# Kernel tuning notes

Measured on AMD Instinct MI355X. Metric: run time of the kernel, lower is better.

Reference implementation:

```python
import jax, jax.numpy as jnp
import numpy as np

N_PARENT = 50000   # parent voxels
C_IN = 256
C_OUT = 256
FANOUT = 8         # children per parent (kernel 2, stride 2 generative conv)
N_TGT = 200000     # number of ground-truth-occupied child indices


def setup_inputs() -> dict:
    key = jax.random.key(0)
    k_fea, k_wup, k_wcls, k_idx = jax.random.split(key, 4)
    fea = jax.random.normal(k_fea, (N_PARENT, C_IN), dtype=jnp.float32)
    W_up = jax.random.normal(k_wup, (FANOUT, C_IN, C_OUT), dtype=jnp.float32) * (1.0 / np.sqrt(C_IN))
    b_up = jnp.zeros((C_OUT,), dtype=jnp.float32)
    W_cls = jax.random.normal(k_wcls, (C_OUT, 1), dtype=jnp.float32) * (1.0 / np.sqrt(C_OUT))
    b_cls = jnp.zeros((1,), dtype=jnp.float32)
    # kernel_map in-indices into the upsampled coordinate set (GT-occupied children)
    target_idx = jax.random.randint(k_idx, (N_TGT,), 0, N_PARENT * FANOUT, dtype=jnp.int64)
    return {"fea": fea, "W_up": W_up, "b_up": b_up, "W_cls": W_cls,
            "b_cls": b_cls, "target_idx": target_idx}


def reference(fea, W_up, b_up, W_cls, b_cls, target_idx):
    # upsample_block: generative transposed sparse conv. Every parent voxel emits
    # FANOUT children, each via its own [C_IN, C_OUT] kernel slice.
    # [N, C_IN] x [K, C_IN, C_OUT] -> [N, K, C_OUT] -> [N*K, C_OUT]
    fea_up = jnp.einsum('nc,kcd->nkd', fea, W_up).reshape(-1, W_up.shape[2]) + b_up
    # classify_block: 1-channel existence logit
    exist = fea_up @ W_cls + b_cls                      # [N*K, 1]
    # keep = exist > 0 (computed under no_grad in torch)
    keep = jax.lax.stop_gradient(exist[:, 0]) > 0       # [N*K] bool
    # kernel_map target scatter: target[curr_in] = 1
    n_up = fea_up.shape[0]
    target = jnp.zeros((n_up,), dtype=jnp.bool_).at[target_idx].set(True)
    keep = keep | target                                # training: keep |= target
    # MinkowskiPruning(fea, keep): jit-compatible masking instead of compaction
    fea_pruned = jnp.where(keep[:, None], fea_up, jnp.zeros((), fea_up.dtype))
    return fea_pruned, exist, target
```

## Files before the change

kernel.cpp:

```cpp
#include <hip/hip_runtime.h>
#include <hip/hip_bf16.h>

#define N_PARENT 50000
#define C_IN     256
#define C_OUT    256
#define FANOUT   8
#define N_TGT    200000
#define N_UP     (N_PARENT * FANOUT)
#define NCOL     (FANOUT * C_OUT)
#define NSTRIP   391
#define NROWS    (NSTRIP * 128)

#define OFF_A    0u
#define OFF_B    (NSTRIP * 65536u)
#define OFF_V    (OFF_B + 16u * 65536u)
#define OFF_EB   (OFF_V + 8192u)
#define OFF_KEEP (OFF_EB + 256u)

typedef __attribute__((ext_vector_type(8))) short short8;
typedef __attribute__((ext_vector_type(4))) float floatx4;

static __device__ __forceinline__ unsigned short f2bf(float f) {
    return __builtin_bit_cast(unsigned short, __float2bfloat16(f));
}

static __device__ __forceinline__ void gload_lds16(const void* gsrc, void* ldsdst) {
    __builtin_amdgcn_global_load_lds(
        (const __attribute__((address_space(1))) unsigned int*)gsrc,
        (__attribute__((address_space(3))) unsigned int*)ldsdst, 16, 0, 0);
}

#define SCHED_BAR() __builtin_amdgcn_sched_barrier(0)
#define SBAR()      __builtin_amdgcn_s_barrier()

__global__ __launch_bounds__(256) void prep_kernel(
        const float* __restrict__ W_up, const float* __restrict__ b_up,
        const float* __restrict__ W_cls, const float* __restrict__ b_cls,
        unsigned char* __restrict__ ws, float* __restrict__ out2) {
    __shared__ float sm[4];
    const int bid = blockIdx.x;
    const int k = bid >> 8, c = bid & 255;
    const int d = threadIdx.x;

    if (d < 49) {
        const int i4 = bid * 49 + d;
        if (i4 < N_UP / 4)
            *(floatx4*)&out2[i4 * 4] = (floatx4){0.f, 0.f, 0.f, 0.f};
    }

    const float w = W_up[((k * 256 + c) * 256) + d];
    const int bn = (k << 1) | (d >> 7);
    const int jr = d & 127;
    const int t  = c >> 5;
    const int ch = (c >> 3) & 3;
    const int e  = c & 7;
    const unsigned off = OFF_B + (unsigned)bn * 65536u + (unsigned)t * 8192u
                       + (unsigned)jr * 64u + (unsigned)((ch ^ (jr & 3)) << 4)
                       + (unsigned)(e << 1);
    *(unsigned short*)(ws + off) = f2bf(w);

    float p = w * W_cls[d];
    #pragma unroll
    for (int m = 1; m < 64; m <<= 1) p += __shfl_xor(p, m);
    if ((d & 63) == 0) sm[d >> 6] = p;
    __syncthreads();
    if (d == 0)
        ((float*)(ws + OFF_V))[k * 256 + c] = sm[0] + sm[1] + sm[2] + sm[3];

    if (bid == 0) {
        __syncthreads();
        float q = b_up[d] * W_cls[d];
        #pragma unroll
        for (int m = 1; m < 64; m <<= 1) q += __shfl_xor(q, m);
        if ((d & 63) == 0) sm[d >> 6] = q;
        __syncthreads();
        if (d == 0)
            *((float*)(ws + OFF_EB)) = sm[0] + sm[1] + sm[2] + sm[3] + b_cls[0];
    }
}

__global__ __launch_bounds__(256) void scatter_kernel(
        const int* __restrict__ idx, float* __restrict__ out2) {
    int i = blockIdx.x * 256 + threadIdx.x;
    if (i < N_TGT) out2[idx[i]] = 1.0f;
}

__global__ __launch_bounds__(256) void convert_kernel(
        const float* __restrict__ fea, const float* __restrict__ target,
        float* __restrict__ out1, unsigned char* __restrict__ ws) {
    const float* V = (const float*)(ws + OFF_V);
    const float eb = *(const float*)(ws + OFF_EB);

    const int rowid = blockIdx.x * 4 + (threadIdx.x >> 6);
    const int lane  = threadIdx.x & 63;
    const bool valid = rowid < N_PARENT;

    floatx4 f = (floatx4){0.f, 0.f, 0.f, 0.f};
    if (valid)
        f = __builtin_nontemporal_load(
                (const floatx4*)&fea[(size_t)rowid * C_IN + lane * 4]);

    float ex[8];
    #pragma unroll
    for (int k = 0; k < 8; ++k) {
        const float4 v = *(const float4*)&V[k * 256 + lane * 4];
        ex[k] = f[0] * v.x + f[1] * v.y + f[2] * v.z + f[3] * v.w;
    }

    const unsigned long long pk =
          (unsigned long long)f2bf(f[0])
        | ((unsigned long long)f2bf(f[1]) << 16)
        | ((unsigned long long)f2bf(f[2]) << 32)
        | ((unsigned long long)f2bf(f[3]) << 48);
    const int strip = rowid >> 7, r = rowid & 127;
    const int t = lane >> 3, ch = (lane >> 1) & 3, half = lane & 1;
    const unsigned off = OFF_A + (unsigned)strip * 65536u + (unsigned)t * 8192u
                       + (unsigned)r * 64u + (unsigned)((ch ^ (r & 3)) << 4)
                       + (unsigned)(half * 8);
    *(unsigned long long*)(ws + off) = pk;

    #pragma unroll
    for (int m = 8; m < 64; m <<= 1)
        #pragma unroll
        for (int k = 0; k < 8; ++k) ex[k] += __shfl_xor(ex[k], m);

    const int ksel = lane >> 3;
    float v = ex[0];
    #pragma unroll
    for (int k = 1; k < 8; ++k) v = (ksel == k) ? ex[k] : v;
    #pragma unroll
    for (int m = 1; m < 8; m <<= 1) v += __shfl_xor(v, m);
    v += eb;

    if ((lane & 7) == 0 && valid) {
        const size_t o = (size_t)rowid * FANOUT + ksel;
        out1[o] = v;
        ws[OFF_KEEP + o] = ((v > 0.0f) || (target[o] != 0.0f)) ? 1 : 0;
    }
}

__global__ __launch_bounds__(256, 4) void gemm_kernel(
        const float* __restrict__ b_up, const unsigned char* __restrict__ ws,
        float* __restrict__ out0) {
    __shared__ unsigned short As[2][4096];
    __shared__ unsigned short Bs[2][4096];
    __shared__ unsigned char keeps[128];

    const int bid = blockIdx.x;
    const int g = bid & 7, u = bid >> 3;
    const int tt = u >> 4, bn = u & 15;
    const int bm = g + 8 * tt;
    if (bm >= NSTRIP) return;

    const unsigned char* Abase = ws + OFF_A + (size_t)bm * 65536u;
    const unsigned char* Bbase = ws + OFF_B + (size_t)bn * 65536u;

    const int tid  = threadIdx.x;
    const int lane = tid & 63;
    const int wid  = tid >> 6;
    const int wr = wid >> 1, wc = wid & 1;
    const int llo = lane & 15, lhi = lane >> 4;

    if (tid < 128) {
        const int n = bm * 128 + tid;
        keeps[tid] = (n < N_PARENT) ? ws[OFF_KEEP + (size_t)n * FANOUT + (bn >> 1)] : 0;
    }

    floatx4 acc[4][4];
    #pragma unroll
    for (int a = 0; a < 4; ++a)
        #pragma unroll
        for (int b = 0; b < 4; ++b) acc[a][b] = (floatx4){0.f, 0.f, 0.f, 0.f};

    #pragma unroll
    for (int t0 = 0; t0 < 2; ++t0) {
        const unsigned o = (unsigned)t0 * 8192u;
        gload_lds16(Abase + o + tid * 16,        (char*)As[t0] + tid * 16);
        gload_lds16(Abase + o + 4096 + tid * 16, (char*)As[t0] + 4096 + tid * 16);
        gload_lds16(Bbase + o + tid * 16,        (char*)Bs[t0] + tid * 16);
        gload_lds16(Bbase + o + 4096 + tid * 16, (char*)Bs[t0] + 4096 + tid * 16);
    }

    #pragma unroll
    for (int t = 0; t < 8; ++t) {
        const int cur = t & 1;

        if (t < 7) asm volatile("s_waitcnt vmcnt(4)" ::: "memory");
        else       asm volatile("s_waitcnt vmcnt(0)" ::: "memory");
        SCHED_BAR();
        SBAR();
        SCHED_BAR();

        short8 af[4], bf[4];
        #pragma unroll
        for (int fm = 0; fm < 4; ++fm) {
            const int row = wr * 64 + fm * 16 + llo;
            const int ch = lhi ^ (row & 3);
            af[fm] = *(const short8*)((const char*)As[cur] + row * 64 + ch * 16);
        }
        #pragma unroll
        for (int fn = 0; fn < 4; ++fn) {
            const int row = wc * 64 + fn * 16 + llo;
            const int ch = lhi ^ (row & 3);
            bf[fn] = *(const short8*)((const char*)Bs[cur] + row * 64 + ch * 16);
        }

        asm volatile("s_waitcnt lgkmcnt(0)" ::: "memory");
        SCHED_BAR();
        SBAR();
        SCHED_BAR();

        if (t < 6) {
            const unsigned o = (unsigned)(t + 2) * 8192u;
            gload_lds16(Abase + o + tid * 16,        (char*)As[cur] + tid * 16);
            gload_lds16(Abase + o + 4096 + tid * 16, (char*)As[cur] + 4096 + tid * 16);
            gload_lds16(Bbase + o + tid * 16,        (char*)Bs[cur] + tid * 16);
            gload_lds16(Bbase + o + 4096 + tid * 16, (char*)Bs[cur] + 4096 + tid * 16);
        }

        #pragma unroll
        for (int fm = 0; fm < 4; ++fm)
            #pragma unroll
            for (int fn = 0; fn < 4; ++fn)
                acc[fm][fn] = __builtin_amdgcn_mfma_f32_16x16x32_bf16(
                    bf[fn], af[fm], acc[fm][fn], 0, 0, 0);
    }

    const int j0 = bn * 128;
    #pragma unroll
    for (int fm = 0; fm < 4; ++fm) {
        const int row = wr * 64 + fm * 16 + llo;
        const int m = bm * 128 + row;
        if (m >= N_PARENT) continue;
        const bool kp = keeps[row] != 0;
        #pragma unroll
        for (int fn = 0; fn < 4; ++fn) {
            const int j = j0 + wc * 64 + fn * 16 + lhi * 4;
            const float4 bv = *(const float4*)&b_up[j & 255];
            const floatx4 a = acc[fm][fn];
            floatx4 o;
            o[0] = kp ? a[0] + bv.x : 0.0f;
            o[1] = kp ? a[1] + bv.y : 0.0f;
            o[2] = kp ? a[2] + bv.z : 0.0f;
            o[3] = kp ? a[3] + bv.w : 0.0f;
            __builtin_nontemporal_store(o, (floatx4*)&out0[(size_t)m * NCOL + j]);
        }
    }
}

extern "C" void kernel_launch(void* const* d_in, const int* in_sizes, int n_in,
                              void* d_out, int out_size, void* d_ws, size_t ws_size,
                              hipStream_t stream) {
    const float* fea   = (const float*)d_in[0];
    const float* W_up  = (const float*)d_in[1];
    const float* b_up  = (const float*)d_in[2];
    const float* W_cls = (const float*)d_in[3];
    const float* b_cls = (const float*)d_in[4];
    const int*   tidx  = (const int*)d_in[5];

    float* out0 = (float*)d_out;
    float* out1 = out0 + (size_t)N_UP * C_OUT;
    float* out2 = out1 + N_UP;
    unsigned char* ws = (unsigned char*)d_ws;

    prep_kernel<<<2048, 256, 0, stream>>>(W_up, b_up, W_cls, b_cls, ws, out2);
    scatter_kernel<<<(N_TGT + 255) / 256, 256, 0, stream>>>(tidx, out2);
    convert_kernel<<<NROWS / 4, 256, 0, stream>>>(fea, out2, out1, ws);
    gemm_kernel<<<392 * 16, 256, 0, stream>>>(b_up, ws, out0);
}
```

Measured before the change: 148.8 us.

## Load GEMM B fragments directly from global memory instead of staging in LDS

The weight (B) operand is now read by each wave straight from the workspace into registers rather than being staged through shared memory. The workspace layout for B drops the XOR swizzle so that each lane's fragment is a contiguous 16-byte chunk. This halves LDS traffic and LDS footprint, which may allow more blocks per CU, and the bias values are hoisted into registers before the main loop. The cost is that the global B loads sit on the critical path: each is waited on before the MFMAs in the same iteration, so it depends on L2 hits and weakens the existing double-buffered prefetch overlap.

```diff
diff --git a/kernel.cpp b/kernel.cpp
--- a/kernel.cpp
+++ b/kernel.cpp
@@ -52,10 +52,10 @@
     const int bn = (k << 1) | (d >> 7);
     const int jr = d & 127;
     const int t  = c >> 5;
-    const int ch = (c >> 3) & 3;
+    const int g  = (c >> 3) & 3;
     const int e  = c & 7;
     const unsigned off = OFF_B + (unsigned)bn * 65536u + (unsigned)t * 8192u
-                       + (unsigned)jr * 64u + (unsigned)((ch ^ (jr & 3)) << 4)
+                       + (unsigned)jr * 64u + (unsigned)(g << 4)
                        + (unsigned)(e << 1);
     *(unsigned short*)(ws + off) = f2bf(w);
 
@@ -143,7 +143,6 @@
         const float* __restrict__ b_up, const unsigned char* __restrict__ ws,
         float* __restrict__ out0) {
     __shared__ unsigned short As[2][4096];
-    __shared__ unsigned short Bs[2][4096];
     __shared__ unsigned char keeps[128];
 
     const int bid = blockIdx.x;
@@ -153,7 +152,6 @@
     if (bm >= NSTRIP) return;
 
     const unsigned char* Abase = ws + OFF_A + (size_t)bm * 65536u;
-    const unsigned char* Bbase = ws + OFF_B + (size_t)bn * 65536u;
 
     const int tid  = threadIdx.x;
     const int lane = tid & 63;
@@ -165,6 +163,13 @@
         const int n = bm * 128 + tid;
         keeps[tid] = (n < N_PARENT) ? ws[OFF_KEEP + (size_t)n * FANOUT + (bn >> 1)] : 0;
     }
+    float4 bv[4];
+    #pragma unroll
+    for (int fn = 0; fn < 4; ++fn)
+        bv[fn] = *(const float4*)&b_up[(bn * 128 + wc * 64 + fn * 16 + lhi * 4) & 255];
+
+    const unsigned char* Bw = ws + OFF_B + (size_t)bn * 65536u
+                            + (unsigned)((wc * 64 + llo) * 64 + lhi * 16);
 
     floatx4 acc[4][4];
     #pragma unroll
@@ -177,33 +182,29 @@
         const unsigned o = (unsigned)t0 * 8192u;
         gload_lds16(Abase + o + tid * 16,        (char*)As[t0] + tid * 16);
         gload_lds16(Abase + o + 4096 + tid * 16, (char*)As[t0] + 4096 + tid * 16);
-        gload_lds16(Bbase + o + tid * 16,        (char*)Bs[t0] + tid * 16);
-        gload_lds16(Bbase + o + 4096 + tid * 16, (char*)Bs[t0] + 4096 + tid * 16);
-    }
+    }
+    asm volatile("s_waitcnt vmcnt(0)" ::: "memory");
+    SCHED_BAR();
 
     #pragma unroll
     for (int t = 0; t < 8; ++t) {
         const int cur = t & 1;
 
-        if (t < 7) asm volatile("s_waitcnt vmcnt(4)" ::: "memory");
-        else       asm volatile("s_waitcnt vmcnt(0)" ::: "memory");
-        SCHED_BAR();
         SBAR();
         SCHED_BAR();
 
-        short8 af[4], bf[4];
+        short8 bf[4];
+        #pragma unroll
+        for (int fn = 0; fn < 4; ++fn)
+            bf[fn] = *(const short8*)(Bw + (unsigned)t * 8192u + fn * 1024);
+
+        short8 af[4];
         #pragma unroll
         for (int fm = 0; fm < 4; ++fm) {
             const int row = wr * 64 + fm * 16 + llo;
             const int ch = lhi ^ (row & 3);
             af[fm] = *(const short8*)((const char*)As[cur] + row * 64 + ch * 16);
         }
-        #pragma unroll
-        for (int fn = 0; fn < 4; ++fn) {
-            const int row = wc * 64 + fn * 16 + llo;
-            const int ch = lhi ^ (row & 3);
-            bf[fn] = *(const short8*)((const char*)Bs[cur] + row * 64 + ch * 16);
-        }
 
         asm volatile("s_waitcnt lgkmcnt(0)" ::: "memory");
         SCHED_BAR();
@@ -214,9 +215,11 @@
             const unsigned o = (unsigned)(t + 2) * 8192u;
             gload_lds16(Abase + o + tid * 16,        (char*)As[cur] + tid * 16);
             gload_lds16(Abase + o + 4096 + tid * 16, (char*)As[cur] + 4096 + tid * 16);
-            gload_lds16(Bbase + o + tid * 16,        (char*)Bs[cur] + tid * 16);
-            gload_lds16(Bbase + o + 4096 + tid * 16, (char*)Bs[cur] + 4096 + tid * 16);
         }
+
+        if (t < 6) asm volatile("s_waitcnt vmcnt(2)" ::: "memory");
+        else       asm volatile("s_waitcnt vmcnt(0)" ::: "memory");
+        SCHED_BAR();
 
         #pragma unroll
         for (int fm = 0; fm < 4; ++fm)
@@ -226,7 +229,6 @@
                     bf[fn], af[fm], acc[fm][fn], 0, 0, 0);
     }
 
-    const int j0 = bn * 128;
     #pragma unroll
     for (int fm = 0; fm < 4; ++fm) {
         const int row = wr * 64 + fm * 16 + llo;
@@ -235,14 +237,13 @@
         const bool kp = keeps[row] != 0;
         #pragma unroll
         for (int fn = 0; fn < 4; ++fn) {
-            const int j = j0 + wc * 64 + fn * 16 + lhi * 4;
-            const float4 bv = *(const float4*)&b_up[j & 255];
+            const int j = bn * 128 + wc * 64 + fn * 16 + lhi * 4;
             const floatx4 a = acc[fm][fn];
             floatx4 o;
-            o[0] = kp ? a[0] + bv.x : 0.0f;
-            o[1] = kp ? a[1] + bv.y : 0.0f;
-            o[2] = kp ? a[2] + bv.z : 0.0f;
-            o[3] = kp ? a[3] + bv.w : 0.0f;
+            o[0] = kp ? a[0] + bv[fn].x : 0.0f;
+            o[1] = kp ? a[1] + bv[fn].y : 0.0f;
+            o[2] = kp ? a[2] + bv[fn].z : 0.0f;
+            o[3] = kp ? a[3] + bv[fn].w : 0.0f;
             __builtin_nontemporal_store(o, (floatx4*)&out0[(size_t)m * NCOL + j]);
         }
     }
```

Result: slower. 161.7 us (+8.7%).
